# Optimization experiments

Hardware: AMD Instinct MI355X
Metric: run time of the kernel (lower is better)

The kernel has to match this reference:

```python
import jax, jax.numpy as jnp
import numpy as np

B = 32      # graphs per batch
N_NODES = 1024  # nodes per graph
K = 16      # top-k edges per node


def setup_inputs() -> dict:
    key = jax.random.key(0)
    k1, k2 = jax.random.split(key)
    x = jax.random.normal(k1, (B * N_NODES, 128), dtype=jnp.float32) * 0.1
    W = jax.random.normal(k2, (128, 64), dtype=jnp.float32) * (1.0 / np.sqrt(128))
    b = jnp.zeros((64,), dtype=jnp.float32)
    temperature = jnp.asarray(4.0, dtype=jnp.float32)
    return {"x": x, "W": W, "b": b, "temperature": temperature}


def reference(x, W, b, temperature):
    # Encoder: linear node embedding. out: [B*n, C]
    out = x @ W + b
    C = out.shape[-1]
    # Per-graph features, detached as in the original (graph_x = out[...].detach())
    h = jax.lax.stop_gradient(out).reshape(B, N_NODES, C)
    # Pairwise squared euclidean distances per graph: d[b,i,j] = ||h_i - h_j||^2
    sq = jnp.sum(h * h, axis=-1)  # [B, n]
    d_e = sq[:, :, None] + sq[:, None, :] - 2.0 * jnp.einsum('bic,bjc->bij', h, h)
    logits = jnp.exp(-temperature * d_e)  # [B, n, n]
    # Gumbel-noised top-k edge sampling
    z = jax.random.gumbel(jax.random.key(1), logits.shape, logits.dtype)
    _, edges_hat = jax.lax.top_k(logits + z, K)  # [B, n, K] int32
    # Build global edge index with cumulative per-graph node offsets
    offsets = (jnp.arange(B, dtype=jnp.int32) * N_NODES)[:, None, None]  # [B,1,1]
    rows = jnp.broadcast_to(jnp.arange(N_NODES, dtype=jnp.int32)[None, :, None] + offsets,
                            (B, N_NODES, K))
    cols = edges_hat.astype(jnp.int32) + offsets
    edges_idx = jnp.stack((rows.reshape(-1), cols.reshape(-1)))  # [2, B*n*K]
    return out, edges_idx
```

## Files before the change

kernel.cpp:

```cpp
#include <hip/hip_runtime.h>
#include <math.h>

#define OUT_ELEMS 2097152
#define EDGE_ELEMS 524288

__device__ __forceinline__ unsigned int rotl32(unsigned int x, int r){
  return (x << r) | (x >> (32 - r));
}

__device__ __forceinline__ unsigned int tf_bits_part(unsigned int e){
  unsigned int x0 = 0u, x1 = e;
  const unsigned int ks1 = 1u;
  const unsigned int ks2 = 0x1BD11BDBu;
  x1 += ks1;
#define TFR(r) { x0 += x1; x1 = rotl32(x1, r); x1 ^= x0; }
  TFR(13) TFR(15) TFR(26) TFR(6)
  x0 += ks1; x1 += ks2 + 1u;
  TFR(17) TFR(29) TFR(16) TFR(24)
  x0 += ks2; x1 += 0u + 2u;
  TFR(13) TFR(15) TFR(26) TFR(6)
  x0 += 0u;  x1 += ks1 + 3u;
  TFR(17) TFR(29) TFR(16) TFR(24)
  x0 += ks1; x1 += ks2 + 4u;
  TFR(13) TFR(15) TFR(26) TFR(6)
  x0 += ks2; x1 += 0u + 5u;
#undef TFR
  return x0 ^ x1;
}

__device__ __forceinline__ double rcp64(double x){
  double r;
  asm("v_rcp_f64 %0, %1" : "=v"(r) : "v"(x));
  double e = fma(-x, r, 1.0); r = fma(r, e, r);
  e = fma(-x, r, 1.0); r = fma(r, e, r);
  return r;
}

__device__ __forceinline__ double fast_exp(double x){
  double fn = __builtin_rint(x * 1.4426950408889634);
  int n = (int)fn;
  double r = fma(fn, -0.6931471803691238, x);
  r = fma(fn, -1.9082149292705877e-10, r);
  double p = 2.7557319223985893e-06;
  p = fma(r, p, 2.4801587301587302e-05);
  p = fma(r, p, 1.9841269841269841e-04);
  p = fma(r, p, 1.3888888888888889e-03);
  p = fma(r, p, 8.3333333333333333e-03);
  p = fma(r, p, 4.1666666666666664e-02);
  p = fma(r, p, 1.6666666666666666e-01);
  p = fma(r, p, 0.5);
  p = fma(r, p, 1.0);
  p = fma(r, p, 1.0);
  double scale = __longlong_as_double(((long long)(n + 1023)) << 52);
  return p * scale;
}

__device__ __forceinline__ double fast_log(double x){
  long long bx = __double_as_longlong(x);
  long long e = (bx >> 52) - 1023;
  double m = __longlong_as_double((bx & 0xFFFFFFFFFFFFFll) |
                                  0x3FF0000000000000ll);
  int big = m > 1.4142135623730951;
  m = big ? 0.5 * m : m;
  e += big;
  double s = (m - 1.0) * rcp64(m + 1.0);
  double s2 = s * s;
  double p = fma(s2, 2.0/11.0, 2.0/9.0);
  p = fma(s2, p, 2.0/7.0);
  p = fma(s2, p, 2.0/5.0);
  p = fma(s2, p, 2.0/3.0);
  double lm = fma(s * s2, p, 2.0 * s);
  return fma((double)e, 0.6931471805599453, lm);
}

__device__ __forceinline__ unsigned long long score_cand(
    const float* __restrict__ og, const double* __restrict__ hrow,
    unsigned int jc, unsigned int base, double Td, bool act){
  const float4* cp4 = (const float4*)(og + ((size_t)jc << 6));
  double acc = 0.0;
  #pragma unroll 4
  for (int ch = 0; ch < 16; ++ch){
    float4 cf = cp4[ch];
    double d0 = hrow[(ch << 2) + 0] - (double)cf.x;
    double d1 = hrow[(ch << 2) + 1] - (double)cf.y;
    double d2 = hrow[(ch << 2) + 2] - (double)cf.z;
    double d3 = hrow[(ch << 2) + 3] - (double)cf.w;
    acc = fma(d0, d0, acc);
    acc = fma(d1, d1, acc);
    acc = fma(d2, d2, acc);
    acc = fma(d3, d3, acc);
  }
  if (!act) return 0ull;
  double sgm = fast_exp(-Td * acc);
  unsigned int bits = tf_bits_part(base | jc);
  float f = __uint_as_float(0x3f800000u | (bits >> 9)) - 1.0f;
  double u = (f > 0.0f) ? (double)f : 1.1754943508222875e-38;
  double w = -fast_log(u);
  double z = -fast_log(w);
  double sc = sgm + z;
  unsigned long long kb = (unsigned long long)__double_as_longlong(sc);
  kb ^= (unsigned long long)(((long long)kb) >> 63) | 0x8000000000000000ull;
  return (kb & ~1023ull) | (unsigned long long)(1023u - jc);
}

__device__ __forceinline__ unsigned long long bitonic64_desc(
    unsigned long long key, int lane){
  #pragma unroll
  for (int k = 2; k <= 64; k <<= 1){
    #pragma unroll
    for (int j = k >> 1; j; j >>= 1){
      unsigned long long o = __shfl_xor(key, j, 64);
      bool keep_hi = ((lane & k) == 0) == ((lane & j) == 0);
      key = (keep_hi == (o > key)) ? o : key;
    }
  }
  return key;
}

__device__ __forceinline__ unsigned int bitonic32_desc(
    unsigned int key, int lane){
  #pragma unroll
  for (int k = 2; k <= 64; k <<= 1){
    #pragma unroll
    for (int j = k >> 1; j; j >>= 1){
      unsigned int o = __shfl_xor(key, j, 64);
      bool keep_hi = ((lane & k) == 0) == ((lane & j) == 0);
      key = (keep_hi == (o > key)) ? o : key;
    }
  }
  return key;
}

__global__ __launch_bounds__(256) void encoder_v10(
    const float* __restrict__ x, const float* __restrict__ W,
    const float* __restrict__ b, float* __restrict__ out){
  __shared__ double xs64[8192];
  const int tid = threadIdx.x;
  const int w = tid >> 6, c = tid & 63;
  const size_t r0 = (size_t)blockIdx.x << 6;

  {
    const float4* xg4 = (const float4*)(x + (r0 << 7));
    #pragma unroll
    for (int s = 0; s < 8; ++s){
      const int idx = tid + (s << 8);
      float4 v = xg4[idx];
      double2 d0, d1;
      d0.x = (double)v.x; d0.y = (double)v.y;
      d1.x = (double)v.z; d1.y = (double)v.w;
      *(double2*)&xs64[(idx << 2) + 0] = d0;
      *(double2*)&xs64[(idx << 2) + 2] = d1;
    }
  }
  __syncthreads();

  double acc[16];
  const double bc = (double)b[c];
  #pragma unroll
  for (int i = 0; i < 16; ++i) acc[i] = bc;

  #pragma unroll 4
  for (int k = 0; k < 128; k += 4){
    const double w0 = (double)W[((k + 0) << 6) + c];
    const double w1 = (double)W[((k + 1) << 6) + c];
    const double w2 = (double)W[((k + 2) << 6) + c];
    const double w3 = (double)W[((k + 3) << 6) + c];
    #pragma unroll
    for (int i = 0; i < 16; ++i){
      const double2 xa = *(const double2*)&xs64[(((w << 4) + i) << 7) + k];
      const double2 xb = *(const double2*)&xs64[(((w << 4) + i) << 7) + k + 2];
      acc[i] = fma(xa.x, w0, acc[i]);
      acc[i] = fma(xa.y, w1, acc[i]);
      acc[i] = fma(xb.x, w2, acc[i]);
      acc[i] = fma(xb.y, w3, acc[i]);
    }
  }
  #pragma unroll
  for (int i = 0; i < 16; ++i)
    out[((r0 + (w << 4) + i) << 6) + c] = (float)acc[i];
}

__global__ __launch_bounds__(256, 8) void edges_v10(
    const float* __restrict__ out32, const float* __restrict__ temp,
    float* __restrict__ rows_out, float* __restrict__ cols_out){
  __shared__ double hid[4][64];
  __shared__ unsigned int cl[4][128];
  const int tid = threadIdx.x, wave = tid >> 6, lane = tid & 63;
  const int gb = blockIdx.x >> 8;
  const int i0 = (blockIdx.x & 255) << 2;
  const int r  = i0 + wave;
  const float* __restrict__ og = out32 + ((size_t)gb << 16);

  hid[wave][lane] = (double)og[((size_t)r << 6) + lane];

  const unsigned int base = ((unsigned int)gb << 20) | ((unsigned int)r << 10);

  unsigned int v[16];
  unsigned int pmax = 0u;
  #pragma unroll
  for (int m = 0; m < 16; ++m){
    const unsigned int j = (unsigned int)(m << 6) + (unsigned int)lane;
    unsigned int bits = tf_bits_part(base | j);
    v[m] = (bits & ~1023u) | (1023u - j);
    pmax = (v[m] > pmax) ? v[m] : pmax;
  }

  unsigned int sorted = bitonic32_desc(pmax, lane);
  unsigned int b16p = __shfl(sorted, 15, 64);

  float u16 = __uint_as_float(0x3f800000u | (b16p >> 9)) - 1.0f;
  float z16 = -__logf(-__logf(u16));
  float uc  = __expf(-__expf(-(z16 - 1.001f)));
  unsigned int cp = ((__float_as_uint(1.0f + uc) & 0x7FFFFFu) << 9) & ~1023u;

  int cnt = 0;
  #pragma unroll
  for (int m = 0; m < 16; ++m) cnt += (v[m] >= cp) ? 1 : 0;
  int s = cnt;
  #pragma unroll
  for (int off = 1; off < 64; off <<= 1){
    int o = __shfl_up(s, off, 64);
    s += (lane >= off) ? o : 0;
  }
  int nc = __shfl(s, 63, 64);
  nc = (nc > 128) ? 128 : nc;
  int slot = s - cnt;
  #pragma unroll
  for (int m = 0; m < 16; ++m){
    if (v[m] >= cp && slot < 128){
      cl[wave][slot] = 1023u - (v[m] & 1023u);
      ++slot;
    }
  }

  const double Td = (double)temp[0];
  const bool act1 = (lane < nc);
  unsigned int jc1 = act1 ? cl[wave][lane] : 0u;
  unsigned long long key = score_cand(og, hid[wave], jc1, base, Td, act1);
  key = bitonic64_desc(key, lane);

  if (nc > 64){
    const int idx2 = 64 + lane;
    const bool act2 = (idx2 < nc);
    unsigned int jc2 = act2 ? cl[wave][idx2] : 0u;
    unsigned long long k2 = score_cand(og, hid[wave], jc2, base, Td, act2);
    k2 = bitonic64_desc(k2, lane);
    unsigned long long kr = __shfl(k2, 63 - lane, 64);
    key = (kr > key) ? kr : key;
    #pragma unroll
    for (int j = 32; j; j >>= 1){
      unsigned long long o = __shfl_xor(key, j, 64);
      bool left = (lane & j) == 0;
      bool take = left ? (o > key) : (o < key);
      key = take ? o : key;
    }
  }

  const int grow = (gb << 10) + r;
  if (lane < 16){
    rows_out[((size_t)grow << 4) + lane] = (float)grow;
    cols_out[((size_t)grow << 4) + lane] =
        (float)((gb << 10) + (1023 - (int)(key & 1023ull)));
  }
}

extern "C" void kernel_launch(void* const* d_in, const int* in_sizes, int n_in,
                              void* d_out, int out_size, void* d_ws, size_t ws_size,
                              hipStream_t stream){
  const float* x = (const float*)d_in[0];
  const float* W = (const float*)d_in[1];
  const float* b = (const float*)d_in[2];
  const float* T = (const float*)d_in[3];
  float* out      = (float*)d_out;
  float* rows_out = out + OUT_ELEMS;
  float* cols_out = rows_out + EDGE_ELEMS;

  encoder_v10<<<512, 256, 0, stream>>>(x, W, b, out);
  edges_v10<<<8192, 256, 0, stream>>>(out, T, rows_out, cols_out);
}
```

Baseline: 194.9 us.

## Move Gumbel candidate prefiltering into encoder kernel via workspace

```diff
diff --git a/kernel.cpp b/kernel.cpp
--- a/kernel.cpp
+++ b/kernel.cpp
@@ -3,6 +3,9 @@
 
 #define OUT_ELEMS 2097152
 #define EDGE_ELEMS 524288
+#define CL_WS_BYTES (32768ull * 128ull * 4ull)
+#define NC_WS_BYTES (32768ull * 4ull)
+#define WS_NEED (CL_WS_BYTES + NC_WS_BYTES)
 
 __device__ __forceinline__ unsigned int rotl32(unsigned int x, int r){
   return (x << r) | (x >> (32 - r));
@@ -131,6 +134,154 @@
   return key;
 }
 
+template<typename P>
+__device__ __forceinline__ int phase123(
+    unsigned int base, int lane, P* clrow){
+  unsigned int v[16];
+  unsigned int pmax = 0u;
+  #pragma unroll
+  for (int m = 0; m < 16; ++m){
+    const unsigned int j = (unsigned int)(m << 6) + (unsigned int)lane;
+    unsigned int bits = tf_bits_part(base | j);
+    v[m] = (bits & ~1023u) | (1023u - j);
+    pmax = (v[m] > pmax) ? v[m] : pmax;
+  }
+  unsigned int sorted = bitonic32_desc(pmax, lane);
+  unsigned int b16p = __shfl(sorted, 15, 64);
+  float u16 = __uint_as_float(0x3f800000u | (b16p >> 9)) - 1.0f;
+  float z16 = -__logf(-__logf(u16));
+  float uc  = __expf(-__expf(-(z16 - 1.001f)));
+  unsigned int cp = ((__float_as_uint(1.0f + uc) & 0x7FFFFFu) << 9) & ~1023u;
+  int cnt = 0;
+  #pragma unroll
+  for (int m = 0; m < 16; ++m) cnt += (v[m] >= cp) ? 1 : 0;
+  int s = cnt;
+  #pragma unroll
+  for (int off = 1; off < 64; off <<= 1){
+    int o = __shfl_up(s, off, 64);
+    s += (lane >= off) ? o : 0;
+  }
+  int nc = __shfl(s, 63, 64);
+  nc = (nc > 128) ? 128 : nc;
+  int slot = s - cnt;
+  #pragma unroll
+  for (int m = 0; m < 16; ++m){
+    if (v[m] >= cp && slot < 128){
+      clrow[slot] = 1023u - (v[m] & 1023u);
+      ++slot;
+    }
+  }
+  return nc;
+}
+
+__device__ __forceinline__ void phase4(
+    const float* __restrict__ og, const double* __restrict__ hrow,
+    unsigned int jc1, unsigned int jc2, bool act1, bool act2, int nc,
+    unsigned int base, double Td, int gb, int grow, int lane,
+    float* __restrict__ rows_out, float* __restrict__ cols_out){
+  unsigned long long key = score_cand(og, hrow, jc1, base, Td, act1);
+  key = bitonic64_desc(key, lane);
+  if (nc > 64){
+    unsigned long long k2 = score_cand(og, hrow, jc2, base, Td, act2);
+    k2 = bitonic64_desc(k2, lane);
+    unsigned long long kr = __shfl(k2, 63 - lane, 64);
+    key = (kr > key) ? kr : key;
+    #pragma unroll
+    for (int j = 32; j; j >>= 1){
+      unsigned long long o = __shfl_xor(key, j, 64);
+      bool left = (lane & j) == 0;
+      bool take = left ? (o > key) : (o < key);
+      key = take ? o : key;
+    }
+  }
+  if (lane < 16){
+    rows_out[((size_t)grow << 4) + lane] = (float)grow;
+    cols_out[((size_t)grow << 4) + lane] =
+        (float)((gb << 10) + (1023 - (int)(key & 1023ull)));
+  }
+}
+
+__global__ __launch_bounds__(256, 8) void encA_v12(
+    const float* __restrict__ x, const float* __restrict__ W,
+    const float* __restrict__ b, float* __restrict__ out,
+    unsigned int* __restrict__ cl_ws, int* __restrict__ nc_ws){
+  __shared__ float xs[2048];
+  const int tid = threadIdx.x, wave = tid >> 6, lane = tid & 63;
+  const int bid = blockIdx.x;
+  const size_t r0 = (size_t)bid << 4;
+  const int gb = bid >> 6;
+  const int lr0 = (bid & 63) << 4;
+
+  {
+    const float4* xg4 = (const float4*)(x + (r0 << 7));
+    float4* xs4 = (float4*)xs;
+    xs4[tid] = xg4[tid];
+    xs4[tid + 256] = xg4[tid + 256];
+  }
+  __syncthreads();
+
+  {
+    double acc[4];
+    const double bc = (double)b[lane];
+    #pragma unroll
+    for (int i = 0; i < 4; ++i) acc[i] = bc;
+    #pragma unroll 4
+    for (int k = 0; k < 128; k += 4){
+      const double w0 = (double)W[((k + 0) << 6) + lane];
+      const double w1 = (double)W[((k + 1) << 6) + lane];
+      const double w2 = (double)W[((k + 2) << 6) + lane];
+      const double w3 = (double)W[((k + 3) << 6) + lane];
+      #pragma unroll
+      for (int i = 0; i < 4; ++i){
+        const float4 xv = *(const float4*)&xs[(((wave << 2) + i) << 7) + k];
+        acc[i] = fma((double)xv.x, w0, acc[i]);
+        acc[i] = fma((double)xv.y, w1, acc[i]);
+        acc[i] = fma((double)xv.z, w2, acc[i]);
+        acc[i] = fma((double)xv.w, w3, acc[i]);
+      }
+    }
+    #pragma unroll
+    for (int i = 0; i < 4; ++i)
+      out[((r0 + (wave << 2) + i) << 6) + lane] = (float)acc[i];
+  }
+
+  #pragma unroll 1
+  for (int rr = 0; rr < 4; ++rr){
+    const int lrow = (wave << 2) + rr;
+    const int grow = (int)r0 + lrow;
+    const unsigned int base =
+        ((unsigned int)gb << 20) | ((unsigned int)(lr0 + lrow) << 10);
+    int nc = phase123(base, lane, cl_ws + ((size_t)grow << 7));
+    if (lane == 0) nc_ws[grow] = nc;
+  }
+}
+
+__global__ __launch_bounds__(256, 8) void p4B_v12(
+    const float* __restrict__ out32, const float* __restrict__ temp,
+    const unsigned int* __restrict__ cl_ws, const int* __restrict__ nc_ws,
+    float* __restrict__ rows_out, float* __restrict__ cols_out){
+  __shared__ double hid[4][64];
+  const int tid = threadIdx.x, wave = tid >> 6, lane = tid & 63;
+  const int gb = blockIdx.x >> 8;
+  const int i0 = (blockIdx.x & 255) << 2;
+  const int r  = i0 + wave;
+  const int grow = (gb << 10) + r;
+  const float* __restrict__ og = out32 + ((size_t)gb << 16);
+
+  hid[wave][lane] = (double)og[((size_t)r << 6) + lane];
+  const unsigned int base = ((unsigned int)gb << 20) | ((unsigned int)r << 10);
+  const int nc = nc_ws[grow];
+  const unsigned int* clg = cl_ws + ((size_t)grow << 7);
+  const bool act1 = (lane < nc);
+  const bool act2 = (64 + lane < nc);
+  unsigned int jc1 = act1 ? clg[lane] : 0u;
+  unsigned int jc2 = act2 ? clg[64 + lane] : 0u;
+  const double Td = (double)temp[0];
+  phase4(og, &hid[wave][0], jc1, jc2, act1, act2, nc, base, Td,
+         gb, grow, lane, rows_out, cols_out);
+}
+
+
 __global__ __launch_bounds__(256) void encoder_v10(
     const float* __restrict__ x, const float* __restrict__ W,
     const float* __restrict__ b, float* __restrict__ out){
@@ -138,7 +289,6 @@
   const int tid = threadIdx.x;
   const int w = tid >> 6, c = tid & 63;
   const size_t r0 = (size_t)blockIdx.x << 6;
-
   {
     const float4* xg4 = (const float4*)(x + (r0 << 7));
     #pragma unroll
@@ -153,12 +303,10 @@
     }
   }
   __syncthreads();
-
   double acc[16];
   const double bc = (double)b[c];
   #pragma unroll
   for (int i = 0; i < 16; ++i) acc[i] = bc;
-
   #pragma unroll 4
   for (int k = 0; k < 128; k += 4){
     const double w0 = (double)W[((k + 0) << 6) + c];
@@ -185,6 +333,7 @@
     float* __restrict__ rows_out, float* __restrict__ cols_out){
   __shared__ double hid[4][64];
   __shared__ unsigned int cl[4][128];
+  __shared__ int ncA[4];
   const int tid = threadIdx.x, wave = tid >> 6, lane = tid & 63;
   const int gb = blockIdx.x >> 8;
   const int i0 = (blockIdx.x & 255) << 2;
@@ -192,76 +341,18 @@
   const float* __restrict__ og = out32 + ((size_t)gb << 16);
 
   hid[wave][lane] = (double)og[((size_t)r << 6) + lane];
-
   const unsigned int base = ((unsigned int)gb << 20) | ((unsigned int)r << 10);
-
-  unsigned int v[16];
-  unsigned int pmax = 0u;
-  #pragma unroll
-  for (int m = 0; m < 16; ++m){
-    const unsigned int j = (unsigned int)(m << 6) + (unsigned int)lane;
-    unsigned int bits = tf_bits_part(base | j);
-    v[m] = (bits & ~1023u) | (1023u - j);
-    pmax = (v[m] > pmax) ? v[m] : pmax;
-  }
-
-  unsigned int sorted = bitonic32_desc(pmax, lane);
-  unsigned int b16p = __shfl(sorted, 15, 64);
-
-  float u16 = __uint_as_float(0x3f800000u | (b16p >> 9)) - 1.0f;
-  float z16 = -__logf(-__logf(u16));
-  float uc  = __expf(-__expf(-(z16 - 1.001f)));
-  unsigned int cp = ((__float_as_uint(1.0f + uc) & 0x7FFFFFu) << 9) & ~1023u;
-
-  int cnt = 0;
-  #pragma unroll
-  for (int m = 0; m < 16; ++m) cnt += (v[m] >= cp) ? 1 : 0;
-  int s = cnt;
-  #pragma unroll
-  for (int off = 1; off < 64; off <<= 1){
-    int o = __shfl_up(s, off, 64);
-    s += (lane >= off) ? o : 0;
-  }
-  int nc = __shfl(s, 63, 64);
-  nc = (nc > 128) ? 128 : nc;
-  int slot = s - cnt;
-  #pragma unroll
-  for (int m = 0; m < 16; ++m){
-    if (v[m] >= cp && slot < 128){
-      cl[wave][slot] = 1023u - (v[m] & 1023u);
-      ++slot;
-    }
-  }
-
+  int nc = phase123(base, lane, &cl[wave][0]);
+  if (lane == 0) ncA[wave] = nc;
   const double Td = (double)temp[0];
-  const bool act1 = (lane < nc);
+  const int grow = (gb << 10) + r;
+  const int ncw = ncA[wave];
+  const bool act1 = (lane < ncw);
+  const bool act2 = (64 + lane < ncw);
   unsigned int jc1 = act1 ? cl[wave][lane] : 0u;
-  unsigned long long key = score_cand(og, hid[wave], jc1, base, Td, act1);
-  key = bitonic64_desc(key, lane);
-
-  if (nc > 64){
-    const int idx2 = 64 + lane;
-    const bool act2 = (idx2 < nc);
-    unsigned int jc2 = act2 ? cl[wave][idx2] : 0u;
-    unsigned long long k2 = score_cand(og, hid[wave], jc2, base, Td, act2);
-    k2 = bitonic64_desc(k2, lane);
-    unsigned long long kr = __shfl(k2, 63 - lane, 64);
-    key = (kr > key) ? kr : key;
-    #pragma unroll
-    for (int j = 32; j; j >>= 1){
-      unsigned long long o = __shfl_xor(key, j, 64);
-      bool left = (lane & j) == 0;
-      bool take = left ? (o > key) : (o < key);
-      key = take ? o : key;
-    }
-  }
-
-  const int grow = (gb << 10) + r;
-  if (lane < 16){
-    rows_out[((size_t)grow << 4) + lane] = (float)grow;
-    cols_out[((size_t)grow << 4) + lane] =
-        (float)((gb << 10) + (1023 - (int)(key & 1023ull)));
-  }
+  unsigned int jc2 = act2 ? cl[wave][64 + lane] : 0u;
+  phase4(og, &hid[wave][0], jc1, jc2, act1, act2, ncw, base, Td,
+         gb, grow, lane, rows_out, cols_out);
 }
 
 extern "C" void kernel_launch(void* const* d_in, const int* in_sizes, int n_in,
@@ -275,6 +366,14 @@
   float* rows_out = out + OUT_ELEMS;
   float* cols_out = rows_out + EDGE_ELEMS;
 
-  encoder_v10<<<512, 256, 0, stream>>>(x, W, b, out);
-  edges_v10<<<8192, 256, 0, stream>>>(out, T, rows_out, cols_out);
-}
+  if (ws_size >= WS_NEED){
+    unsigned int* cl_ws = (unsigned int*)d_ws;
+    int* nc_ws = (int*)((char*)d_ws + CL_WS_BYTES);
+    encA_v12<<<2048, 256, 0, stream>>>(x, W, b, out, cl_ws, nc_ws);
+    p4B_v12<<<8192, 256, 0, stream>>>(out, T, cl_ws, nc_ws,
+                                      rows_out, cols_out);
+  } else {
+    encoder_v10<<<512, 256, 0, stream>>>(x, W, b, out);
+    edges_v10<<<8192, 256, 0, stream>>>(out, T, rows_out, cols_out);
+  }
+}
```

After: 247.3 us. 1.27x slower.
